# Kernel optimization log

Measured on AMD Instinct MI355X. Metric: run time of the kernel, lower is better.

The kernel has to match this reference:

```python
import jax, jax.numpy as jnp
import numpy as np

B, S, D, T = 64, 512, 768, 9  # batch, seq_len, bert hidden, tag_size


def setup_inputs() -> dict:
    key = jax.random.key(0)
    ks = jax.random.split(key, 7)
    return {
        "embeds": jax.random.normal(ks[0], (B, S, D), jnp.float32),          # frozen BERT output
        "weight": jax.random.normal(ks[1], (T, D), jnp.float32) * 0.02,      # nn.Linear(768, tag_size)
        "bias": jnp.zeros((T,), jnp.float32),
        "start_transitions": jax.random.normal(ks[2], (T,), jnp.float32) * 0.1,
        "end_transitions": jax.random.normal(ks[3], (T,), jnp.float32) * 0.1,
        "transitions": jax.random.normal(ks[4], (T, T), jnp.float32) * 0.1,
        "tags": jax.random.randint(ks[5], (B, S), 0, T),
        "mask": jnp.ones((B, S), bool),  # torchcrf requires mask[:, 0] all on
    }


def reference(embeds, weight, bias, start_transitions, end_transitions, transitions, tags, mask):
    # Linear emission head (dropout is identity at eval)
    emissions = jnp.einsum("bsd,td->bst", embeds, weight) + bias  # [B,S,T]
    maskf = mask.astype(emissions.dtype)

    # --- numerator: score of gold path (torchcrf _compute_score) ---
    emit = jnp.take_along_axis(emissions, tags[:, :, None], axis=2)[:, :, 0]  # [B,S]
    trans = transitions[tags[:, :-1], tags[:, 1:]]                            # [B,S-1]
    num = start_transitions[tags[:, 0]] + emit[:, 0]
    num = num + jnp.sum((trans + emit[:, 1:]) * maskf[:, 1:], axis=1)
    seq_ends = jnp.sum(mask.astype(jnp.int32), axis=1) - 1                    # [B]
    last_tags = jnp.take_along_axis(tags, seq_ends[:, None], axis=1)[:, 0]
    num = num + end_transitions[last_tags]

    # --- denominator: forward algorithm (torchcrf _compute_normalizer) ---
    def step(score, xs):
        e_t, m_t = xs  # [B,T], [B]
        nxt = jax.nn.logsumexp(score[:, :, None] + transitions[None] + e_t[:, None, :], axis=1)
        return jnp.where(m_t[:, None], nxt, score), None

    score0 = start_transitions[None, :] + emissions[:, 0]                     # [B,T]
    xs = (jnp.swapaxes(emissions[:, 1:], 0, 1), jnp.swapaxes(mask[:, 1:], 0, 1))
    score, _ = jax.lax.scan(step, score0, xs)
    den = jax.nn.logsumexp(score + end_transitions[None, :], axis=1)          # [B]

    llh = num - den
    return -jnp.mean(llh)  # reduction='mean', negated
```

## Files before the change

### kernel.cpp

```cpp
#include <hip/hip_runtime.h>

#define BB 64
#define SS 512
#define DD 768
#define TT 9
#define CC 64
#define LL 8
#define EMSTRIDE 76

template <int CTRL>
__device__ __forceinline__ float dpp_radd(float v) {
  return v + __int_as_float(__builtin_amdgcn_update_dpp(
                 0, __float_as_int(v), CTRL, 0xF, 0xF, true));
}
__device__ __forceinline__ float wave_sum_dpp(float v) {
  v = dpp_radd<0x111>(v);
  v = dpp_radd<0x112>(v);
  v = dpp_radd<0x114>(v);
  v = dpp_radd<0x118>(v);
  v = dpp_radd<0x142>(v);
  v = dpp_radd<0x143>(v);
  return v;
}

__global__ __launch_bounds__(512) void k1_fused(
    const float* __restrict__ embeds, const float* __restrict__ weight,
    const float* __restrict__ bias, const float* __restrict__ startt,
    const float* __restrict__ trans, const int* __restrict__ tags,
    float* __restrict__ colM, float* __restrict__ numpart,
    int* __restrict__ ctr) {
  const int tid  = threadIdx.x;
  const int lane = tid & 63;
  const int wv   = tid >> 6;
  const int b    = blockIdx.x >> 3;
  const int cg   = blockIdx.x & 7;

  if (blockIdx.x == 0 && tid == 0) ctr[0] = 0;

  __shared__ float em[8 * EMSTRIDE];
  __shared__ float trl[81];
  __shared__ float etl[81];
  if (tid < 81) {
    const float tv = trans[tid];
    trl[tid] = tv;
    etl[tid] = __expf(tv);
  }

  float wreg[TT][12];
#pragma unroll
  for (int t = 0; t < TT; ++t) {
#pragma unroll
    for (int k = 0; k < 3; ++k) {
      const float4 v = *(const float4*)(weight + t * DD + k * 256 + lane * 4);
      wreg[t][k * 4 + 0] = v.x; wreg[t][k * 4 + 1] = v.y;
      wreg[t][k * 4 + 2] = v.z; wreg[t][k * 4 + 3] = v.w;
    }
  }
  float bb[TT];
#pragma unroll
  for (int t = 0; t < TT; ++t) bb[t] = bias[t];

  const int row0 = b * SS + cg * 64 + wv * 8;
#pragma unroll
  for (int r = 0; r < LL; ++r) {
    const float* ep = embeds + (size_t)(row0 + r) * DD;
    float e[12];
#pragma unroll
    for (int k = 0; k < 3; ++k) {
      const float4 v = *(const float4*)(ep + k * 256 + lane * 4);
      e[k * 4 + 0] = v.x; e[k * 4 + 1] = v.y;
      e[k * 4 + 2] = v.z; e[k * 4 + 3] = v.w;
    }
    float acc[TT];
#pragma unroll
    for (int t = 0; t < TT; ++t) {
      float a = 0.f;
#pragma unroll
      for (int kk = 0; kk < 12; ++kk) a = fmaf(e[kk], wreg[t][kk], a);
      acc[t] = wave_sum_dpp(a);
    }
    if (lane == 63) {
#pragma unroll
      for (int t = 0; t < TT; ++t)
        em[wv * EMSTRIDE + r * TT + t] = acc[t] + bb[t];
    }
  }
  __syncthreads();

  if (wv == 2) {
    const int sl = lane;
    const int s  = cg * 64 + sl;
    const int* tg = tags + (size_t)b * SS;
    const int tt = tg[s];
    float nterm = em[(sl >> 3) * EMSTRIDE + (sl & 7) * TT + tt];
    nterm += (s == 0) ? startt[tt] : trl[tg[s - 1] * TT + tt];
    nterm = wave_sum_dpp(nterm);
    if (lane == 63) numpart[b * 8 + cg] = nterm;
  }

  if (tid < 8 * TT) {
    const int cl = tid / TT, j = tid % TT;
    const int gc = cg * 8 + cl;
    const float* e = em + cl * EMSTRIDE;

    float v[TT];
#pragma unroll
    for (int i = 0; i < TT; ++i) v[i] = trl[i * TT + j] + e[(LL - 1) * TT + j];

#pragma unroll
    for (int ss = LL - 2; ss >= 0; --ss) {
      float x[TT];
#pragma unroll
      for (int k = 0; k < TT; ++k) x[k] = e[ss * TT + k] + v[k];
      if (ss == 0 && gc == 0) {
#pragma unroll
        for (int k = 0; k < TT; ++k) x[k] += startt[k];
        float m = x[0];
#pragma unroll
        for (int k = 1; k < TT; ++k) m = fmaxf(m, x[k]);
        float sum = 0.f;
#pragma unroll
        for (int k = 0; k < TT; ++k) sum += __expf(x[k] - m);
        const float val = m + __logf(sum);
#pragma unroll
        for (int i = 0; i < TT; ++i) v[i] = val;
      } else {
        float m = x[0];
#pragma unroll
        for (int k = 1; k < TT; ++k) m = fmaxf(m, x[k]);
        float p[TT];
#pragma unroll
        for (int k = 0; k < TT; ++k) p[k] = __expf(x[k] - m);
#pragma unroll
        for (int i = 0; i < TT; ++i) {
          float sum = 0.f;
#pragma unroll
          for (int k = 0; k < TT; ++k) sum = fmaf(etl[i * TT + k], p[k], sum);
          v[i] = m + __logf(sum);
        }
      }
    }
    float* out = colM + ((size_t)(b * CC + gc) * TT + j) * TT;
#pragma unroll
    for (int i = 0; i < TT; ++i) out[i] = v[i];
  }
}

__global__ __launch_bounds__(576) void k2_combine_fin(
    const float* __restrict__ colM, const float* __restrict__ numpart,
    const float* __restrict__ endt, const int* __restrict__ tags,
    float* __restrict__ partial, int* __restrict__ ctr,
    float* __restrict__ out) {
  const int b   = blockIdx.x;
  const int tid = threadIdx.x;
  __shared__ float A[CC * 81];
  __shared__ float Bm[(CC / 2) * 81];

  const float4* src4 = (const float4*)(colM + (size_t)b * CC * 81);
  float4* A4 = (float4*)A;
  for (int q = tid; q < (CC * 81) / 4; q += 576) A4[q] = src4[q];
  __syncthreads();

  float* srcb = A;
  float* dstb = Bm;
  for (int n = CC / 2; n >= 1; n >>= 1) {
    if (tid < n * TT) {
      const int p = tid / TT, j = tid % TT;
      float a[81], wv[TT];
      const float* AT = srcb + (2 * p) * 81;
      const float* BT = srcb + (2 * p + 1) * 81;
#pragma unroll
      for (int q = 0; q < 81; ++q) a[q] = AT[q];
#pragma unroll
      for (int k = 0; k < TT; ++k) wv[k] = BT[j * TT + k];
      float* OT = dstb + p * 81;
#pragma unroll
      for (int i = 0; i < TT; ++i) {
        float x[TT];
#pragma unroll
        for (int k = 0; k < TT; ++k) x[k] = a[k * TT + i] + wv[k];
        float m = x[0];
#pragma unroll
        for (int k = 1; k < TT; ++k) m = fmaxf(m, x[k]);
        float sum = 0.f;
#pragma unroll
        for (int k = 0; k < TT; ++k) sum += __expf(x[k] - m);
        OT[j * TT + i] = m + __logf(sum);
      }
    }
    __syncthreads();
    float* tmp = srcb; srcb = dstb; dstb = tmp;
  }

  if (tid == 0) {
    const int* tg = tags + (size_t)b * SS;
    float num = 0.f;
#pragma unroll
    for (int q = 0; q < 8; ++q) num += numpart[b * 8 + q];
    num += endt[tg[SS - 1]];

    float x[TT];
#pragma unroll
    for (int j = 0; j < TT; ++j) x[j] = srcb[j * TT + 0] + endt[j];
    float m = x[0];
#pragma unroll
    for (int j = 1; j < TT; ++j) m = fmaxf(m, x[j]);
    float sum = 0.f;
#pragma unroll
    for (int j = 0; j < TT; ++j) sum += __expf(x[j] - m);
    partial[b] = (m + __logf(sum)) - num;

    __threadfence();
    const int old = atomicAdd(ctr, 1);
    if (old == BB - 1) {
      __threadfence();
      volatile const float* vp = partial;
      float s = 0.f;
#pragma unroll
      for (int i = 0; i < BB; ++i) s += vp[i];
      out[0] = s * (1.0f / BB);
    }
  }
}

extern "C" void kernel_launch(void* const* d_in, const int* in_sizes, int n_in,
                              void* d_out, int out_size, void* d_ws, size_t ws_size,
                              hipStream_t stream) {
  const float* embeds = (const float*)d_in[0];
  const float* weight = (const float*)d_in[1];
  const float* bias   = (const float*)d_in[2];
  const float* startt = (const float*)d_in[3];
  const float* endt   = (const float*)d_in[4];
  const float* trans  = (const float*)d_in[5];
  const int*   tags   = (const int*)d_in[6];

  float* ws      = (float*)d_ws;
  float* colM    = ws;
  float* numpart = colM + (size_t)BB * CC * 81;
  float* partial = numpart + BB * 8;
  int*   ctr     = (int*)(partial + BB);
  float* out     = (float*)d_out;

  k1_fused<<<BB * 8, 512, 0, stream>>>(embeds, weight, bias, startt, trans,
                                       tags, colM, numpart, ctr);
  k2_combine_fin<<<BB, 576, 0, stream>>>(colM, numpart, endt, tags, partial,
                                         ctr, out);
}
```

Before: 48.97 us.

## Split fused emission/CRF kernel into separate emission, chunk-scan and combine kernels

Splits the fused kernel in two. A dedicated emission GEMV kernel stages the weights in shared memory and processes 4 rows per wave, giving more memory-level parallelism, and writes emissions to global memory. A separate CRF chunk kernel with one thread per (batch, chunk, tag) then builds the per-chunk transition matrices. The gold-path numerator moves into the combine kernel. This aims to raise occupancy and embed-read bandwidth in the dominant GEMV, at the cost of an extra launch and a round-trip of the emissions through global memory.

```diff
diff --git a/kernel.cpp b/kernel.cpp
--- a/kernel.cpp
+++ b/kernel.cpp
@@ -6,7 +6,7 @@
 #define TT 9
 #define CC 64
 #define LL 8
-#define EMSTRIDE 76
+#define RG 4
 
 template <int CTRL>
 __device__ __forceinline__ float dpp_radd(float v) {
@@ -23,131 +23,144 @@
   return v;
 }
 
-__global__ __launch_bounds__(512) void k1_fused(
+__global__ __launch_bounds__(256, 4) void emis_kernel(
     const float* __restrict__ embeds, const float* __restrict__ weight,
-    const float* __restrict__ bias, const float* __restrict__ startt,
-    const float* __restrict__ trans, const int* __restrict__ tags,
-    float* __restrict__ colM, float* __restrict__ numpart,
+    const float* __restrict__ bias, float* __restrict__ emis,
     int* __restrict__ ctr) {
   const int tid  = threadIdx.x;
   const int lane = tid & 63;
   const int wv   = tid >> 6;
-  const int b    = blockIdx.x >> 3;
-  const int cg   = blockIdx.x & 7;
 
   if (blockIdx.x == 0 && tid == 0) ctr[0] = 0;
 
-  __shared__ float em[8 * EMSTRIDE];
-  __shared__ float trl[81];
-  __shared__ float etl[81];
-  if (tid < 81) {
-    const float tv = trans[tid];
-    trl[tid] = tv;
-    etl[tid] = __expf(tv);
-  }
-
-  float wreg[TT][12];
-#pragma unroll
-  for (int t = 0; t < TT; ++t) {
-#pragma unroll
-    for (int k = 0; k < 3; ++k) {
-      const float4 v = *(const float4*)(weight + t * DD + k * 256 + lane * 4);
-      wreg[t][k * 4 + 0] = v.x; wreg[t][k * 4 + 1] = v.y;
-      wreg[t][k * 4 + 2] = v.z; wreg[t][k * 4 + 3] = v.w;
-    }
-  }
-  float bb[TT];
-#pragma unroll
-  for (int t = 0; t < TT; ++t) bb[t] = bias[t];
-
-  const int row0 = b * SS + cg * 64 + wv * 8;
-#pragma unroll
-  for (int r = 0; r < LL; ++r) {
+  __shared__ float wl[TT * DD];
+  __shared__ float bl[TT];
+  {
+    const float4* ws4 = (const float4*)weight;
+    float4* wl4 = (float4*)wl;
+    for (int q = tid; q < (TT * DD) / 4; q += 256) wl4[q] = ws4[q];
+    if (tid < TT) bl[tid] = bias[tid];
+  }
+  __syncthreads();
+
+  const int grp  = blockIdx.x * 4 + wv;
+  const int row0 = grp * RG;
+
+  float e[RG][12];
+#pragma unroll
+  for (int r = 0; r < RG; ++r) {
     const float* ep = embeds + (size_t)(row0 + r) * DD;
-    float e[12];
 #pragma unroll
     for (int k = 0; k < 3; ++k) {
       const float4 v = *(const float4*)(ep + k * 256 + lane * 4);
-      e[k * 4 + 0] = v.x; e[k * 4 + 1] = v.y;
-      e[k * 4 + 2] = v.z; e[k * 4 + 3] = v.w;
-    }
-    float acc[TT];
-#pragma unroll
-    for (int t = 0; t < TT; ++t) {
+      e[r][k * 4 + 0] = v.x; e[r][k * 4 + 1] = v.y;
+      e[r][k * 4 + 2] = v.z; e[r][k * 4 + 3] = v.w;
+    }
+  }
+
+  float acc[RG][TT];
+#pragma unroll
+  for (int t = 0; t < TT; ++t) {
+    float w[12];
+#pragma unroll
+    for (int k = 0; k < 3; ++k) {
+      const float4 v = *(const float4*)(wl + t * DD + k * 256 + lane * 4);
+      w[k * 4 + 0] = v.x; w[k * 4 + 1] = v.y;
+      w[k * 4 + 2] = v.z; w[k * 4 + 3] = v.w;
+    }
+#pragma unroll
+    for (int r = 0; r < RG; ++r) {
       float a = 0.f;
 #pragma unroll
-      for (int kk = 0; kk < 12; ++kk) a = fmaf(e[kk], wreg[t][kk], a);
-      acc[t] = wave_sum_dpp(a);
-    }
-    if (lane == 63) {
+      for (int kk = 0; kk < 12; ++kk) a = fmaf(e[r][kk], w[kk], a);
+      acc[r][t] = a;
+    }
+  }
+
+#pragma unroll
+  for (int r = 0; r < RG; ++r)
+#pragma unroll
+    for (int t = 0; t < TT; ++t) acc[r][t] = wave_sum_dpp(acc[r][t]);
+
+  if (lane == 63) {
+#pragma unroll
+    for (int r = 0; r < RG; ++r)
 #pragma unroll
       for (int t = 0; t < TT; ++t)
-        em[wv * EMSTRIDE + r * TT + t] = acc[t] + bb[t];
-    }
-  }
-  __syncthreads();
-
-  if (wv == 2) {
-    const int sl = lane;
-    const int s  = cg * 64 + sl;
-    const int* tg = tags + (size_t)b * SS;
-    const int tt = tg[s];
-    float nterm = em[(sl >> 3) * EMSTRIDE + (sl & 7) * TT + tt];
-    nterm += (s == 0) ? startt[tt] : trl[tg[s - 1] * TT + tt];
-    nterm = wave_sum_dpp(nterm);
-    if (lane == 63) numpart[b * 8 + cg] = nterm;
-  }
-
-  if (tid < 8 * TT) {
-    const int cl = tid / TT, j = tid % TT;
-    const int gc = cg * 8 + cl;
-    const float* e = em + cl * EMSTRIDE;
-
-    float v[TT];
-#pragma unroll
-    for (int i = 0; i < TT; ++i) v[i] = trl[i * TT + j] + e[(LL - 1) * TT + j];
-
-#pragma unroll
-    for (int ss = LL - 2; ss >= 0; --ss) {
-      float x[TT];
-#pragma unroll
-      for (int k = 0; k < TT; ++k) x[k] = e[ss * TT + k] + v[k];
-      if (ss == 0 && gc == 0) {
-#pragma unroll
-        for (int k = 0; k < TT; ++k) x[k] += startt[k];
-        float m = x[0];
-#pragma unroll
-        for (int k = 1; k < TT; ++k) m = fmaxf(m, x[k]);
+        emis[(size_t)(row0 + r) * TT + t] = acc[r][t] + bl[t];
+  }
+}
+
+__global__ __launch_bounds__(64) void crf_chunk_kernel(
+    const float* __restrict__ emis, const float* __restrict__ trans,
+    const float* __restrict__ startt, float* __restrict__ colM) {
+  const int t = blockIdx.x * 64 + threadIdx.x;
+  const int b = t / (CC * TT);
+  const int r = t % (CC * TT);
+  const int c = r / TT;
+  const int j = r % TT;
+
+  float et[TT][TT];
+#pragma unroll
+  for (int i = 0; i < TT; ++i)
+#pragma unroll
+    for (int k = 0; k < TT; ++k)
+      et[i][k] = __expf(trans[i * TT + k]);
+
+  float e[LL * TT];
+  const float* eb = emis + (size_t)(b * SS + c * LL) * TT;
+#pragma unroll
+  for (int q = 0; q < (LL * TT) / 4; ++q) {
+    const float4 v = *(const float4*)(eb + q * 4);
+    e[q * 4 + 0] = v.x; e[q * 4 + 1] = v.y;
+    e[q * 4 + 2] = v.z; e[q * 4 + 3] = v.w;
+  }
+
+  float v[TT];
+#pragma unroll
+  for (int i = 0; i < TT; ++i) v[i] = trans[i * TT + j] + e[(LL - 1) * TT + j];
+
+#pragma unroll
+  for (int ss = LL - 2; ss >= 0; --ss) {
+    float x[TT];
+#pragma unroll
+    for (int k = 0; k < TT; ++k) x[k] = e[ss * TT + k] + v[k];
+    if (ss == 0 && c == 0) {
+#pragma unroll
+      for (int k = 0; k < TT; ++k) x[k] += startt[k];
+      float m = x[0];
+#pragma unroll
+      for (int k = 1; k < TT; ++k) m = fmaxf(m, x[k]);
+      float sum = 0.f;
+#pragma unroll
+      for (int k = 0; k < TT; ++k) sum += __expf(x[k] - m);
+      const float val = m + __logf(sum);
+#pragma unroll
+      for (int i = 0; i < TT; ++i) v[i] = val;
+    } else {
+      float m = x[0];
+#pragma unroll
+      for (int k = 1; k < TT; ++k) m = fmaxf(m, x[k]);
+      float p[TT];
+#pragma unroll
+      for (int k = 0; k < TT; ++k) p[k] = __expf(x[k] - m);
+#pragma unroll
+      for (int i = 0; i < TT; ++i) {
         float sum = 0.f;
 #pragma unroll
-        for (int k = 0; k < TT; ++k) sum += __expf(x[k] - m);
-        const float val = m + __logf(sum);
-#pragma unroll
-        for (int i = 0; i < TT; ++i) v[i] = val;
-      } else {
-        float m = x[0];
-#pragma unroll
-        for (int k = 1; k < TT; ++k) m = fmaxf(m, x[k]);
-        float p[TT];
-#pragma unroll
-        for (int k = 0; k < TT; ++k) p[k] = __expf(x[k] - m);
-#pragma unroll
-        for (int i = 0; i < TT; ++i) {
-          float sum = 0.f;
-#pragma unroll
-          for (int k = 0; k < TT; ++k) sum = fmaf(etl[i * TT + k], p[k], sum);
-          v[i] = m + __logf(sum);
-        }
+        for (int k = 0; k < TT; ++k) sum = fmaf(et[i][k], p[k], sum);
+        v[i] = m + __logf(sum);
       }
     }
-    float* out = colM + ((size_t)(b * CC + gc) * TT + j) * TT;
-#pragma unroll
-    for (int i = 0; i < TT; ++i) out[i] = v[i];
-  }
-}
-
-__global__ __launch_bounds__(576) void k2_combine_fin(
-    const float* __restrict__ colM, const float* __restrict__ numpart,
+  }
+  float* out = colM + ((size_t)(b * CC + c) * TT + j) * TT;
+#pragma unroll
+  for (int i = 0; i < TT; ++i) out[i] = v[i];
+}
+
+__global__ __launch_bounds__(576) void combine_kernel(
+    const float* __restrict__ colM, const float* __restrict__ emis,
+    const float* __restrict__ trans, const float* __restrict__ startt,
     const float* __restrict__ endt, const int* __restrict__ tags,
     float* __restrict__ partial, int* __restrict__ ctr,
     float* __restrict__ out) {
@@ -155,10 +168,22 @@
   const int tid = threadIdx.x;
   __shared__ float A[CC * 81];
   __shared__ float Bm[(CC / 2) * 81];
+  __shared__ float red2[16];
 
   const float4* src4 = (const float4*)(colM + (size_t)b * CC * 81);
   float4* A4 = (float4*)A;
   for (int q = tid; q < (CC * 81) / 4; q += 576) A4[q] = src4[q];
+
+  const float* E  = emis + (size_t)b * SS * TT;
+  const int*   tg = tags + (size_t)b * SS;
+  float nsum = 0.f;
+  if (tid < SS) {
+    const int tt = tg[tid];
+    nsum = E[tid * TT + tt];
+    nsum += (tid == 0) ? startt[tt] : trans[tg[tid - 1] * TT + tt];
+  }
+  nsum = wave_sum_dpp(nsum);
+  if ((tid & 63) == 63) red2[tid >> 6] = nsum;
   __syncthreads();
 
   float* srcb = A;
@@ -193,10 +218,9 @@
   }
 
   if (tid == 0) {
-    const int* tg = tags + (size_t)b * SS;
-    float num = 0.f;
-#pragma unroll
-    for (int q = 0; q < 8; ++q) num += numpart[b * 8 + q];
+    float num = red2[0];
+#pragma unroll
+    for (int w = 1; w < 9; ++w) num += red2[w];
     num += endt[tg[SS - 1]];
 
     float x[TT];
@@ -235,14 +259,14 @@
   const int*   tags   = (const int*)d_in[6];
 
   float* ws      = (float*)d_ws;
-  float* colM    = ws;
-  float* numpart = colM + (size_t)BB * CC * 81;
-  float* partial = numpart + BB * 8;
+  float* emis    = ws;
+  float* colM    = emis + (size_t)BB * SS * TT;
+  float* partial = colM + (size_t)BB * CC * 81;
   int*   ctr     = (int*)(partial + BB);
   float* out     = (float*)d_out;
 
-  k1_fused<<<BB * 8, 512, 0, stream>>>(embeds, weight, bias, startt, trans,
-                                       tags, colM, numpart, ctr);
-  k2_combine_fin<<<BB, 576, 0, stream>>>(colM, numpart, endt, tags, partial,
-                                         ctr, out);
-}
+  emis_kernel<<<2048, 256, 0, stream>>>(embeds, weight, bias, emis, ctr);
+  crf_chunk_kernel<<<(BB * CC * TT) / 64, 64, 0, stream>>>(emis, trans, startt, colM);
+  combine_kernel<<<BB, 576, 0, stream>>>(colM, emis, trans, startt, endt, tags,
+                                         partial, ctr, out);
+}
```

Measured after the change: 87.25 us. 1.78x slower.

## Merge emission GEMV and CRF reduction into one kernel with grid barrier

Applied to the files above, without the earlier changes.

Replaces the two-kernel pipeline with one persistent kernel. All 512 blocks compute emissions into a global workspace, then signal an atomic counter, and the first 64 blocks spin until every block has arrived. Each of those 64 blocks then does the whole per-batch chunk scan and log-semiring tree reduction in shared memory. This removes a kernel launch boundary and the colM round-trip, but adds a memset, a spin-wait grid barrier that assumes all blocks are co-resident, and less parallelism in the per-batch phase.

```diff
diff --git a/kernel.cpp b/kernel.cpp
--- a/kernel.cpp
+++ b/kernel.cpp
@@ -6,7 +6,8 @@
 #define TT 9
 #define CC 64
 #define LL 8
-#define EMSTRIDE 76
+#define NBLK 512
+#define RPW 16
 
 template <int CTRL>
 __device__ __forceinline__ float dpp_radd(float v) {
@@ -23,96 +24,116 @@
   return v;
 }
 
-__global__ __launch_bounds__(512) void k1_fused(
+__global__ __launch_bounds__(256, 2) void bertcrf_fused(
     const float* __restrict__ embeds, const float* __restrict__ weight,
     const float* __restrict__ bias, const float* __restrict__ startt,
-    const float* __restrict__ trans, const int* __restrict__ tags,
-    float* __restrict__ colM, float* __restrict__ numpart,
-    int* __restrict__ ctr) {
+    const float* __restrict__ endt, const float* __restrict__ trans,
+    const int* __restrict__ tags, float* __restrict__ emis,
+    float* __restrict__ partial, int* __restrict__ ctr,
+    float* __restrict__ out) {
   const int tid  = threadIdx.x;
   const int lane = tid & 63;
   const int wv   = tid >> 6;
-  const int b    = blockIdx.x >> 3;
-  const int cg   = blockIdx.x & 7;
-
-  if (blockIdx.x == 0 && tid == 0) ctr[0] = 0;
-
-  __shared__ float em[8 * EMSTRIDE];
-  __shared__ float trl[81];
-  __shared__ float etl[81];
+
+  __shared__ float em[SS * TT];
+  __shared__ float cm[CC * 81];
+  __shared__ float Bm[(CC / 2) * 81];
+  __shared__ float trl[81], etl[81];
+  __shared__ float red2[4];
+
+  {
+    float w[TT][12];
+#pragma unroll
+    for (int t = 0; t < TT; ++t) {
+#pragma unroll
+      for (int k = 0; k < 3; ++k) {
+        const float4 v = *(const float4*)(weight + t * DD + k * 256 + lane * 4);
+        w[t][k * 4 + 0] = v.x; w[t][k * 4 + 1] = v.y;
+        w[t][k * 4 + 2] = v.z; w[t][k * 4 + 3] = v.w;
+      }
+    }
+    float bb[TT];
+#pragma unroll
+    for (int t = 0; t < TT; ++t) bb[t] = bias[t];
+
+    const int wid = blockIdx.x * 4 + wv;
+#pragma unroll 2
+    for (int r = 0; r < RPW; ++r) {
+      const int row = wid * RPW + r;
+      const float* ep = embeds + (size_t)row * DD;
+      float e[12];
+#pragma unroll
+      for (int k = 0; k < 3; ++k) {
+        const float4 v = *(const float4*)(ep + k * 256 + lane * 4);
+        e[k * 4 + 0] = v.x; e[k * 4 + 1] = v.y;
+        e[k * 4 + 2] = v.z; e[k * 4 + 3] = v.w;
+      }
+      float acc[TT];
+#pragma unroll
+      for (int t = 0; t < TT; ++t) {
+        float a = 0.f;
+#pragma unroll
+        for (int kk = 0; kk < 12; ++kk) a = fmaf(e[kk], w[t][kk], a);
+        acc[t] = wave_sum_dpp(a);
+      }
+      if (lane == 63) {
+#pragma unroll
+        for (int t = 0; t < TT; ++t)
+          emis[(size_t)row * TT + t] = acc[t] + bb[t];
+      }
+    }
+  }
+
+  __syncthreads();
+  __threadfence();
+  if (tid == 0) __hip_atomic_fetch_add(&ctr[0], 1, __ATOMIC_ACQ_REL,
+                                       __HIP_MEMORY_SCOPE_AGENT);
+  if (blockIdx.x >= BB) return;
+
+  if (tid == 0) {
+    while (__hip_atomic_load(&ctr[0], __ATOMIC_ACQUIRE,
+                             __HIP_MEMORY_SCOPE_AGENT) < NBLK) {
+    }
+  }
+  __syncthreads();
+  __threadfence();
+
+  const int b = blockIdx.x;
   if (tid < 81) {
     const float tv = trans[tid];
     trl[tid] = tv;
     etl[tid] = __expf(tv);
   }
-
-  float wreg[TT][12];
-#pragma unroll
-  for (int t = 0; t < TT; ++t) {
-#pragma unroll
-    for (int k = 0; k < 3; ++k) {
-      const float4 v = *(const float4*)(weight + t * DD + k * 256 + lane * 4);
-      wreg[t][k * 4 + 0] = v.x; wreg[t][k * 4 + 1] = v.y;
-      wreg[t][k * 4 + 2] = v.z; wreg[t][k * 4 + 3] = v.w;
-    }
-  }
-  float bb[TT];
-#pragma unroll
-  for (int t = 0; t < TT; ++t) bb[t] = bias[t];
-
-  const int row0 = b * SS + cg * 64 + wv * 8;
-#pragma unroll
-  for (int r = 0; r < LL; ++r) {
-    const float* ep = embeds + (size_t)(row0 + r) * DD;
-    float e[12];
-#pragma unroll
-    for (int k = 0; k < 3; ++k) {
-      const float4 v = *(const float4*)(ep + k * 256 + lane * 4);
-      e[k * 4 + 0] = v.x; e[k * 4 + 1] = v.y;
-      e[k * 4 + 2] = v.z; e[k * 4 + 3] = v.w;
-    }
-    float acc[TT];
-#pragma unroll
-    for (int t = 0; t < TT; ++t) {
-      float a = 0.f;
-#pragma unroll
-      for (int kk = 0; kk < 12; ++kk) a = fmaf(e[kk], wreg[t][kk], a);
-      acc[t] = wave_sum_dpp(a);
-    }
-    if (lane == 63) {
-#pragma unroll
-      for (int t = 0; t < TT; ++t)
-        em[wv * EMSTRIDE + r * TT + t] = acc[t] + bb[t];
-    }
-  }
-  __syncthreads();
-
-  if (wv == 2) {
-    const int sl = lane;
-    const int s  = cg * 64 + sl;
-    const int* tg = tags + (size_t)b * SS;
+  {
+    const float4* e0 = (const float4*)(emis + (size_t)b * SS * TT);
+    float4* em4 = (float4*)em;
+    for (int q = tid; q < (SS * TT) / 4; q += 256) em4[q] = e0[q];
+  }
+  __syncthreads();
+
+  const int* tg = tags + (size_t)b * SS;
+  float nsum = 0.f;
+  for (int s = tid; s < SS; s += 256) {
     const int tt = tg[s];
-    float nterm = em[(sl >> 3) * EMSTRIDE + (sl & 7) * TT + tt];
-    nterm += (s == 0) ? startt[tt] : trl[tg[s - 1] * TT + tt];
-    nterm = wave_sum_dpp(nterm);
-    if (lane == 63) numpart[b * 8 + cg] = nterm;
-  }
-
-  if (tid < 8 * TT) {
-    const int cl = tid / TT, j = tid % TT;
-    const int gc = cg * 8 + cl;
-    const float* e = em + cl * EMSTRIDE;
-
+    float term = em[s * TT + tt];
+    term += (s == 0) ? startt[tt] : trl[tg[s - 1] * TT + tt];
+    nsum += term;
+  }
+  nsum = wave_sum_dpp(nsum);
+  if ((tid & 63) == 63) red2[tid >> 6] = nsum;
+
+  for (int task = tid; task < CC * TT; task += 256) {
+    const int c = task / TT, j = task - (task / TT) * TT;
+    const float* e = em + c * (LL * TT);
     float v[TT];
 #pragma unroll
     for (int i = 0; i < TT; ++i) v[i] = trl[i * TT + j] + e[(LL - 1) * TT + j];
-
 #pragma unroll
     for (int ss = LL - 2; ss >= 0; --ss) {
       float x[TT];
 #pragma unroll
       for (int k = 0; k < TT; ++k) x[k] = e[ss * TT + k] + v[k];
-      if (ss == 0 && gc == 0) {
+      if (ss == 0 && c == 0) {
 #pragma unroll
         for (int k = 0; k < TT; ++k) x[k] += startt[k];
         float m = x[0];
@@ -140,45 +161,29 @@
         }
       }
     }
-    float* out = colM + ((size_t)(b * CC + gc) * TT + j) * TT;
-#pragma unroll
-    for (int i = 0; i < TT; ++i) out[i] = v[i];
-  }
-}
-
-__global__ __launch_bounds__(576) void k2_combine_fin(
-    const float* __restrict__ colM, const float* __restrict__ numpart,
-    const float* __restrict__ endt, const int* __restrict__ tags,
-    float* __restrict__ partial, int* __restrict__ ctr,
-    float* __restrict__ out) {
-  const int b   = blockIdx.x;
-  const int tid = threadIdx.x;
-  __shared__ float A[CC * 81];
-  __shared__ float Bm[(CC / 2) * 81];
-
-  const float4* src4 = (const float4*)(colM + (size_t)b * CC * 81);
-  float4* A4 = (float4*)A;
-  for (int q = tid; q < (CC * 81) / 4; q += 576) A4[q] = src4[q];
-  __syncthreads();
-
-  float* srcb = A;
+#pragma unroll
+    for (int i = 0; i < TT; ++i) cm[c * 81 + j * TT + i] = v[i];
+  }
+  __syncthreads();
+
+  float* srcb = cm;
   float* dstb = Bm;
   for (int n = CC / 2; n >= 1; n >>= 1) {
-    if (tid < n * TT) {
-      const int p = tid / TT, j = tid % TT;
-      float a[81], wv[TT];
+    for (int task = tid; task < n * TT; task += 256) {
+      const int p = task / TT, j = task - (task / TT) * TT;
+      float a[81], wvv[TT];
       const float* AT = srcb + (2 * p) * 81;
       const float* BT = srcb + (2 * p + 1) * 81;
 #pragma unroll
       for (int q = 0; q < 81; ++q) a[q] = AT[q];
 #pragma unroll
-      for (int k = 0; k < TT; ++k) wv[k] = BT[j * TT + k];
+      for (int k = 0; k < TT; ++k) wvv[k] = BT[j * TT + k];
       float* OT = dstb + p * 81;
 #pragma unroll
       for (int i = 0; i < TT; ++i) {
         float x[TT];
 #pragma unroll
-        for (int k = 0; k < TT; ++k) x[k] = a[k * TT + i] + wv[k];
+        for (int k = 0; k < TT; ++k) x[k] = a[k * TT + i] + wvv[k];
         float m = x[0];
 #pragma unroll
         for (int k = 1; k < TT; ++k) m = fmaxf(m, x[k]);
@@ -193,10 +198,7 @@
   }
 
   if (tid == 0) {
-    const int* tg = tags + (size_t)b * SS;
-    float num = 0.f;
-#pragma unroll
-    for (int q = 0; q < 8; ++q) num += numpart[b * 8 + q];
+    float num = red2[0] + red2[1] + red2[2] + red2[3];
     num += endt[tg[SS - 1]];
 
     float x[TT];
@@ -211,7 +213,8 @@
     partial[b] = (m + __logf(sum)) - num;
 
     __threadfence();
-    const int old = atomicAdd(ctr, 1);
+    const int old = __hip_atomic_fetch_add(&ctr[1], 1, __ATOMIC_ACQ_REL,
+                                           __HIP_MEMORY_SCOPE_AGENT);
     if (old == BB - 1) {
       __threadfence();
       volatile const float* vp = partial;
@@ -235,14 +238,12 @@
   const int*   tags   = (const int*)d_in[6];
 
   float* ws      = (float*)d_ws;
-  float* colM    = ws;
-  float* numpart = colM + (size_t)BB * CC * 81;
-  float* partial = numpart + BB * 8;
+  float* emis    = ws;
+  float* partial = emis + (size_t)BB * SS * TT;
   int*   ctr     = (int*)(partial + BB);
   float* out     = (float*)d_out;
 
-  k1_fused<<<BB * 8, 512, 0, stream>>>(embeds, weight, bias, startt, trans,
-                                       tags, colM, numpart, ctr);
-  k2_combine_fin<<<BB, 576, 0, stream>>>(colM, numpart, endt, tags, partial,
-                                         ctr, out);
-}
+  hipMemsetAsync(ctr, 0, 2 * sizeof(int), stream);
+  bertcrf_fused<<<NBLK, 256, 0, stream>>>(embeds, weight, bias, startt, endt,
+                                          trans, tags, emis, partial, ctr, out);
+}
```

After: 120.5 us. 146% more time.
